# Kernel optimization log

Hardware: AMD Instinct MI355X
Metric: run time of the kernel (lower is better)

Reference implementation:

```python
import jax, jax.numpy as jnp
import numpy as np

N_NODES = 10000
N_EDGES = 160000
D = 256
L = 2
EPS = 1e-5


def setup_inputs() -> dict:
    key = jax.random.key(0)
    ks = jax.random.split(key, 12)
    s = 0.05  # weight init scale to keep activations tame
    return {
        "node_h": jax.random.normal(ks[0], (N_NODES, D), jnp.float32),
        "edge_h": jax.random.normal(ks[1], (N_EDGES, D), jnp.float32),
        "src": jax.random.randint(ks[2], (N_EDGES,), 0, N_NODES, jnp.int32),
        "dst": jax.random.randint(ks[3], (N_EDGES,), 0, N_NODES, jnp.int32),
        "Kw": jax.random.normal(ks[4], (L, 2 * D, D), jnp.float32) * s,
        "Kb": jnp.zeros((L, D), jnp.float32),
        "Vw": jax.random.normal(ks[5], (L, 2 * D, D), jnp.float32) * s,
        "Vb": jnp.zeros((L, D), jnp.float32),
        "Qw": jax.random.normal(ks[6], (L, D, D), jnp.float32) * s,
        "Qb": jnp.zeros((L, D), jnp.float32),
        "Ww": jax.random.normal(ks[7], (L, 2 * D, D), jnp.float32) * s,
        "Wb": jnp.zeros((L, D), jnp.float32),
        "Ew": jax.random.normal(ks[8], (L, 3 * D, D), jnp.float32) * s,
        "Eb": jnp.zeros((L, D), jnp.float32),
        "ln_g": jnp.ones((D,), jnp.float32),
        "ln_b": jnp.zeros((D,), jnp.float32),
    }


def _layernorm(x, g, b):
    mu = jnp.mean(x, axis=-1, keepdims=True)
    var = jnp.mean(jnp.square(x - mu), axis=-1, keepdims=True)
    return (x - mu) * jax.lax.rsqrt(var + EPS) * g + b


def _hypergraph_layer(h_n, h_e, src, dst, Kw, Kb, Vw, Vb, Qw, Qb, Ww, Wb, Ew, Eb):
    n = h_n.shape[0]
    src_h = h_n[src]                                   # [E, D] gather
    msg = jnp.concatenate([src_h * h_e, src_h], axis=1)  # [E, 2D]
    Q = h_n @ Qw + Qb                                  # [N, D]
    K = msg @ Kw + Kb                                  # [E, D]
    V = msg @ Vw + Vb                                  # [E, D]
    alpha = Q[dst] * K                                 # v_mul_e -> [E, D]
    # edge_softmax: per-destination-node, per-feature softmax over edges
    m = jax.ops.segment_max(alpha, dst, num_segments=n)
    e = jnp.exp(alpha - m[dst])
    z = jax.ops.segment_sum(e, dst, num_segments=n)
    a = e / z[dst]
    agg = jax.ops.segment_sum(a * V, dst, num_segments=n)  # sum aggregation [N, D]
    h_n_new = jnp.concatenate([agg, h_n], axis=1) @ Ww + Wb
    h_e_new = jnp.concatenate([h_n_new[src], h_n_new[dst], h_e], axis=1) @ Ew + Eb
    return h_n_new, h_e_new


def reference(node_h, edge_h, src, dst, Kw, Kb, Vw, Vb, Qw, Qb, Ww, Wb, Ew, Eb, ln_g, ln_b):
    h_n, h_e = node_h, edge_h
    for l in range(L):  # small fixed layer count
        h_n, h_e = _hypergraph_layer(h_n, h_e, src, dst,
                                     Kw[l], Kb[l], Vw[l], Vb[l], Qw[l], Qb[l],
                                     Ww[l], Wb[l], Ew[l], Eb[l])
        # relu -> layernorm; dropout is identity in eval mode
        h_n = _layernorm(jax.nn.relu(h_n), ln_g, ln_b)
        h_e = _layernorm(jax.nn.relu(h_e), ln_g, ln_b)
    return h_n, h_e
```

## Files before the change

### kernel.cpp

```cpp
#include <hip/hip_runtime.h>

#define NN 10000
#define NE 160000
#define DD 256
#define LEPS 1e-5f

typedef __attribute__((ext_vector_type(8))) short short8v;
typedef __attribute__((ext_vector_type(4))) float floatx4;
typedef unsigned short US;

static __device__ __forceinline__ US f2bf(float f){
  unsigned u = __builtin_bit_cast(unsigned, f);
  u += 0x7FFFu + ((u >> 16) & 1u);
  return (US)(u >> 16);
}
static __device__ __forceinline__ float bf2f(US s){
  unsigned u = ((unsigned)s) << 16;
  return __builtin_bit_cast(float, u);
}
template<typename T>
static __device__ __forceinline__ void ld8(const T* p, float* o){
  if constexpr (sizeof(T) == 2) {
    union { US h[8]; uint4 q; } u;
    u.q = *(const uint4*)p;
#pragma unroll
    for (int j = 0; j < 8; ++j) o[j] = bf2f(u.h[j]);
  } else {
    float4 a = *(const float4*)p; float4 b = *(const float4*)(p + 4);
    o[0]=a.x; o[1]=a.y; o[2]=a.z; o[3]=a.w; o[4]=b.x; o[5]=b.y; o[6]=b.z; o[7]=b.w;
  }
}
template<typename OT>
static __device__ __forceinline__ void st1(OT* p, float v){
  if constexpr (sizeof(OT) == 2) *p = (OT)f2bf(v); else *p = (OT)v;
}
static __device__ __forceinline__ uint4 pack8(const float* a){
  union { US h[8]; uint4 q; } pk;
#pragma unroll
  for (int j = 0; j < 8; ++j) pk.h[j] = f2bf(a[j]);
  return pk.q;
}

#define AOFF_Q  0
#define AOFF_K1 (32*2048)
#define AOFF_K2 (64*2048)
#define AOFF_V1 (96*2048)
#define AOFF_V2 (128*2048)
#define AOFF_W  (160*2048)
#define AOFF_E1 (224*2048)
#define AOFF_E2 (256*2048)
#define AOFF_E3 (288*2048)
__global__ void pack_all_k(const float* __restrict__ Qw, const float* __restrict__ Kw,
                           const float* __restrict__ Vw, const float* __restrict__ Ww,
                           const float* __restrict__ Ew, US* __restrict__ arena){
  int i = blockIdx.x * 256 + threadIdx.x;
  int g = i >> 8, n = i & 255;
  const float* src; int row0;
  if      (g <  32){ src = Qw; row0 = g*8; }
  else if (g <  64){ src = Kw; row0 = (g-32)*8; }
  else if (g <  96){ src = Kw; row0 = 256 + (g-64)*8; }
  else if (g < 128){ src = Vw; row0 = (g-96)*8; }
  else if (g < 160){ src = Vw; row0 = 256 + (g-128)*8; }
  else if (g < 224){ src = Ww; row0 = (g-160)*8; }
  else if (g < 256){ src = Ew; row0 = (g-224)*8; }
  else if (g < 288){ src = Ew; row0 = 256 + (g-256)*8; }
  else             { src = Ew; row0 = 512 + (g-288)*8; }
  union { US h[8]; uint4 q; } pk;
#pragma unroll
  for (int j = 0; j < 8; ++j) pk.h[j] = f2bf(src[(size_t)(row0 + j)*DD + n]);
  *(uint4*)(arena + (size_t)g*2048 + n*8) = pk.q;
}

template<typename AT, typename OT>
__global__ __launch_bounds__(256, 2)
void gemm_nmulti_k(const AT* __restrict__ p0,
                   const US* bp0, const float* b0, OT* o0,
                   const US* bp1, const float* b1, OT* o1,
                   const US* bp2, const float* b2, OT* o2, int M)
{
  const US* Bp  = (blockIdx.y == 0) ? bp0 : (blockIdx.y == 1 ? bp1 : bp2);
  const float* bias = (blockIdx.y == 0) ? b0 : (blockIdx.y == 1 ? b1 : b2);
  OT* out = (blockIdx.y == 0) ? o0 : (blockIdx.y == 1 ? o1 : o2);
  __shared__ __align__(16) US Alds[64][40];
  __shared__ __align__(16) US Blds[8192];
  const int tid  = threadIdx.x;
  const int lane = tid & 63;
  const int wav  = tid >> 6;
  const int bm   = blockIdx.x * 64;

  floatx4 acc[4][4];
#pragma unroll
  for (int i = 0; i < 4; ++i)
#pragma unroll
    for (int j = 0; j < 4; ++j) acc[i][j] = (floatx4){0.f,0.f,0.f,0.f};

  const int ar = tid >> 2;
  const int ak = (tid & 3) << 3;
  int grow = bm + ar; if (grow > M - 1) grow = M - 1;
  const AT* rA = p0 + (size_t)grow * DD;
  const int rq = lane >> 4;
  const int cl = lane & 15;

  uint4 arow[8];
#pragma unroll
  for (int t = 0; t < 8; ++t) {
    float av[8]; ld8(rA + t*32 + ak, av);
    arow[t] = pack8(av);
  }

  for (int t = 0; t < 8; ++t) {
    *(uint4*)&Alds[ar][ak] = arow[t];
    const uint4* bsrc = (const uint4*)(Bp + (size_t)(t*4) * 2048);
    uint4* bdst = (uint4*)Blds;
#pragma unroll
    for (int u = 0; u < 4; ++u) bdst[tid + u*256] = bsrc[tid + u*256];
    __syncthreads();

    short8v af[4], bfr[4];
#pragma unroll
    for (int i = 0; i < 4; ++i) af[i] = *(const short8v*)&Alds[i*16 + cl][rq*8];
#pragma unroll
    for (int j = 0; j < 4; ++j) bfr[j] = *(const short8v*)&Blds[(size_t)(rq*256 + wav*64 + j*16 + cl) * 8];
#pragma unroll
    for (int i = 0; i < 4; ++i)
#pragma unroll
      for (int j = 0; j < 4; ++j)
        acc[i][j] = __builtin_amdgcn_mfma_f32_16x16x32_bf16(af[i], bfr[j], acc[i][j], 0, 0, 0);
    __syncthreads();
  }

#pragma unroll
  for (int i = 0; i < 4; ++i)
#pragma unroll
    for (int r = 0; r < 4; ++r) {
      int gm = bm + i*16 + rq*4 + r;
      if (gm < M) {
#pragma unroll
        for (int j = 0; j < 4; ++j) {
          int n = wav*64 + j*16 + cl;
          float b = bias ? bias[n] : 0.f;
          st1(out + (size_t)gm*DD + n, acc[i][j][r] + b);
        }
      }
    }
}

template<typename AT, typename OT>
__global__ __launch_bounds__(256, 2)
void gemm_w_k(const float* __restrict__ p0, const AT* __restrict__ p1,
              const US* __restrict__ Bp, const float* __restrict__ bias,
              const float* __restrict__ lg, const float* __restrict__ lb,
              float* __restrict__ Craw, OT* __restrict__ Cln, int M)
{
  __shared__ __align__(16) US Alds[64][40];
  __shared__ __align__(16) US Blds[8192];
  __shared__ float S1[4][64], S2[4][64];
  const int tid  = threadIdx.x;
  const int lane = tid & 63;
  const int wav  = tid >> 6;
  const int bm   = blockIdx.x * 64;

  floatx4 acc[4][4];
#pragma unroll
  for (int i = 0; i < 4; ++i)
#pragma unroll
    for (int j = 0; j < 4; ++j) acc[i][j] = (floatx4){0.f,0.f,0.f,0.f};

  const int ar = tid >> 2;
  const int ak = (tid & 3) << 3;
  int grow = bm + ar; if (grow > M - 1) grow = M - 1;
  const float* rA = p0 + (size_t)grow * DD;
  const AT*    rB = p1 + (size_t)grow * DD;
  const int rq = lane >> 4;
  const int cl = lane & 15;

  uint4 arow[16];
#pragma unroll
  for (int t = 0; t < 16; ++t) {
    const int kk = t*32 + ak;
    float av[8];
    if (kk < DD) ld8(rA + kk, av); else ld8(rB + kk - DD, av);
    arow[t] = pack8(av);
  }

  for (int t = 0; t < 16; ++t) {
    *(uint4*)&Alds[ar][ak] = arow[t];
    const uint4* bsrc = (const uint4*)(Bp + (size_t)(t*4) * 2048);
    uint4* bdst = (uint4*)Blds;
#pragma unroll
    for (int u = 0; u < 4; ++u) bdst[tid + u*256] = bsrc[tid + u*256];
    __syncthreads();

    short8v af[4], bfr[4];
#pragma unroll
    for (int i = 0; i < 4; ++i) af[i] = *(const short8v*)&Alds[i*16 + cl][rq*8];
#pragma unroll
    for (int j = 0; j < 4; ++j) bfr[j] = *(const short8v*)&Blds[(size_t)(rq*256 + wav*64 + j*16 + cl) * 8];
#pragma unroll
    for (int i = 0; i < 4; ++i)
#pragma unroll
      for (int j = 0; j < 4; ++j)
        acc[i][j] = __builtin_amdgcn_mfma_f32_16x16x32_bf16(af[i], bfr[j], acc[i][j], 0, 0, 0);
    __syncthreads();
  }

#pragma unroll
  for (int i = 0; i < 4; ++i)
#pragma unroll
    for (int j = 0; j < 4; ++j) {
      int n = wav*64 + j*16 + cl;
      float bs = bias[n];
#pragma unroll
      for (int r = 0; r < 4; ++r) {
        int gm = bm + i*16 + rq*4 + r;
        float val = acc[i][j][r] + bs;
        if (gm < M) Craw[(size_t)gm*DD + n] = val;
        acc[i][j][r] = fmaxf(val, 0.f);
      }
    }
#pragma unroll
  for (int i = 0; i < 4; ++i)
#pragma unroll
    for (int r = 0; r < 4; ++r) {
      float s1 = 0.f, s2 = 0.f;
#pragma unroll
      for (int j = 0; j < 4; ++j){ float v = acc[i][j][r]; s1 += v; s2 += v*v; }
#pragma unroll
      for (int o = 1; o < 16; o <<= 1){ s1 += __shfl_xor(s1, o, 64); s2 += __shfl_xor(s2, o, 64); }
      if (cl == 0){ S1[wav][i*16 + rq*4 + r] = s1; S2[wav][i*16 + rq*4 + r] = s2; }
    }
  __syncthreads();
#pragma unroll
  for (int i = 0; i < 4; ++i)
#pragma unroll
    for (int r = 0; r < 4; ++r) {
      int rr = i*16 + rq*4 + r;
      float t1 = S1[0][rr] + S1[1][rr] + S1[2][rr] + S1[3][rr];
      float t2 = S2[0][rr] + S2[1][rr] + S2[2][rr] + S2[3][rr];
      float mu = t1 * (1.f/256.f);
      float var = t2 * (1.f/256.f) - mu*mu;
      float rs = rsqrtf(fmaxf(var, 0.f) + LEPS);
      int gm = bm + i*16 + rq*4 + r;
      if (gm < M) {
#pragma unroll
        for (int j = 0; j < 4; ++j) {
          int n = wav*64 + j*16 + cl;
          st1(Cln + (size_t)gm*DD + n, (acc[i][j][r] - mu) * rs * lg[n] + lb[n]);
        }
      }
    }
}

template<typename AT>
__global__ __launch_bounds__(256, 2)
void gemm_kve_k(const AT* __restrict__ p0, const AT* __restrict__ p1,
                const int* __restrict__ srcI,
                const US* __restrict__ BpK, const US* __restrict__ BpV,
                const US* __restrict__ KN, const US* __restrict__ VN,
                const int* __restrict__ eperm,
                US* __restrict__ Km, US* __restrict__ Vm, int M)
{
  __shared__ __align__(16) US Alds[64][40];
  __shared__ __align__(16) US BldsK[8192];
  __shared__ __align__(16) US BldsV[8192];
  const int tid  = threadIdx.x;
  const int lane = tid & 63;
  const int wav  = tid >> 6;
  const int bm   = blockIdx.x * 64;

  floatx4 accK[4][4], accV[4][4];
#pragma unroll
  for (int i = 0; i < 4; ++i)
#pragma unroll
    for (int j = 0; j < 4; ++j){ accK[i][j] = (floatx4){0.f,0.f,0.f,0.f}; accV[i][j] = (floatx4){0.f,0.f,0.f,0.f}; }

  const int ar = tid >> 2;
  const int ak = (tid & 3) << 3;
  int grow = bm + ar; if (grow > M - 1) grow = M - 1;
  int s = srcI[grow];
  const AT* rA = p0 + (size_t)s * DD;
  const AT* rB = p1 + (size_t)grow * DD;
  const int rq = lane >> 4;
  const int cl = lane & 15;

  uint4 msg[8];
#pragma unroll
  for (int t = 0; t < 8; ++t) {
    const int kk = t*32 + ak;
    float av[8], bv[8];
    ld8(rA + kk, av); ld8(rB + kk, bv);
    float mv[8];
#pragma unroll
    for (int j = 0; j < 8; ++j) mv[j] = av[j] * bv[j];
    msg[t] = pack8(mv);
  }

  for (int t = 0; t < 8; ++t) {
    *(uint4*)&Alds[ar][ak] = msg[t];
    const uint4* bsK = (const uint4*)(BpK + (size_t)(t*4) * 2048);
    const uint4* bsV = (const uint4*)(BpV + (size_t)(t*4) * 2048);
    uint4* bdK = (uint4*)BldsK; uint4* bdV = (uint4*)BldsV;
#pragma unroll
    for (int u = 0; u < 4; ++u){ bdK[tid + u*256] = bsK[tid + u*256]; bdV[tid + u*256] = bsV[tid + u*256]; }
    __syncthreads();

    short8v af[4], bK4[4], bV4[4];
#pragma unroll
    for (int i = 0; i < 4; ++i) af[i] = *(const short8v*)&Alds[i*16 + cl][rq*8];
#pragma unroll
    for (int j = 0; j < 4; ++j){
      size_t bi = (size_t)(rq*256 + wav*64 + j*16 + cl) * 8;
      bK4[j] = *(const short8v*)&BldsK[bi];
      bV4[j] = *(const short8v*)&BldsV[bi];
    }
#pragma unroll
    for (int i = 0; i < 4; ++i)
#pragma unroll
      for (int j = 0; j < 4; ++j){
        accK[i][j] = __builtin_amdgcn_mfma_f32_16x16x32_bf16(af[i], bK4[j], accK[i][j], 0, 0, 0);
        accV[i][j] = __builtin_amdgcn_mfma_f32_16x16x32_bf16(af[i], bV4[j], accV[i][j], 0, 0, 0);
      }
    __syncthreads();
  }

#pragma unroll
  for (int i = 0; i < 4; ++i)
#pragma unroll
    for (int r = 0; r < 4; ++r) {
      int gm = bm + i*16 + rq*4 + r;
      if (gm < M) {
        int pg = eperm[gm];
        int sg = srcI[gm];
        const US* kn = KN + (size_t)sg * DD;
        const US* vn = VN + (size_t)sg * DD;
#pragma unroll
        for (int j = 0; j < 4; ++j) {
          int n = wav*64 + j*16 + cl;
          Km[(size_t)pg*DD + n] = f2bf(accK[i][j][r] + bf2f(kn[n]));
          Vm[(size_t)pg*DD + n] = f2bf(accV[i][j][r] + bf2f(vn[n]));
        }
      }
    }
}

template<typename AT, typename OT>
__global__ __launch_bounds__(256, 2)
void gemm_e_k(const AT* __restrict__ he, const int* __restrict__ srcI,
              const int* __restrict__ dstI, const US* __restrict__ Bp,
              const US* __restrict__ EN1, const US* __restrict__ EN2,
              const float* __restrict__ lg, const float* __restrict__ lb,
              OT* __restrict__ Cln, int M)
{
  __shared__ __align__(16) US Alds[64][40];
  __shared__ __align__(16) US Blds[8192];
  __shared__ float S1[4][64], S2[4][64];
  const int tid  = threadIdx.x;
  const int lane = tid & 63;
  const int wav  = tid >> 6;
  const int bm   = blockIdx.x * 64;

  floatx4 acc[4][4];
#pragma unroll
  for (int i = 0; i < 4; ++i)
#pragma unroll
    for (int j = 0; j < 4; ++j) acc[i][j] = (floatx4){0.f,0.f,0.f,0.f};

  const int ar = tid >> 2;
  const int ak = (tid & 3) << 3;
  int grow = bm + ar; if (grow > M - 1) grow = M - 1;
  const AT* rA = he + (size_t)grow * DD;
  const int rq = lane >> 4;
  const int cl = lane & 15;

  uint4 arow[8];
#pragma unroll
  for (int t = 0; t < 8; ++t) {
    float av[8]; ld8(rA + t*32 + ak, av);
    arow[t] = pack8(av);
  }

  for (int t = 0; t < 8; ++t) {
    *(uint4*)&Alds[ar][ak] = arow[t];
    const uint4* bsrc = (const uint4*)(Bp + (size_t)(t*4) * 2048);
    uint4* bdst = (uint4*)Blds;
#pragma unroll
    for (int u = 0; u < 4; ++u) bdst[tid + u*256] = bsrc[tid + u*256];
    __syncthreads();

    short8v af[4], bfr[4];
#pragma unroll
    for (int i = 0; i < 4; ++i) af[i] = *(const short8v*)&Alds[i*16 + cl][rq*8];
#pragma unroll
    for (int j = 0; j < 4; ++j) bfr[j] = *(const short8v*)&Blds[(size_t)(rq*256 + wav*64 + j*16 + cl) * 8];
#pragma unroll
    for (int i = 0; i < 4; ++i)
#pragma unroll
      for (int j = 0; j < 4; ++j)
        acc[i][j] = __builtin_amdgcn_mfma_f32_16x16x32_bf16(af[i], bfr[j], acc[i][j], 0, 0, 0);
    __syncthreads();
  }

#pragma unroll
  for (int i = 0; i < 4; ++i)
#pragma unroll
    for (int r = 0; r < 4; ++r) {
      int gm = bm + i*16 + rq*4 + r;
      int gmc = (gm < M) ? gm : (M - 1);
      const US* e1 = EN1 + (size_t)srcI[gmc] * DD;
      const US* e2 = EN2 + (size_t)dstI[gmc] * DD;
#pragma unroll
      for (int j = 0; j < 4; ++j) {
        int n = wav*64 + j*16 + cl;
        float val = acc[i][j][r] + bf2f(e1[n]) + bf2f(e2[n]);
        acc[i][j][r] = fmaxf(val, 0.f);
      }
    }
#pragma unroll
  for (int i = 0; i < 4; ++i)
#pragma unroll
    for (int r = 0; r < 4; ++r) {
      float s1 = 0.f, s2 = 0.f;
#pragma unroll
      for (int j = 0; j < 4; ++j){ float v = acc[i][j][r]; s1 += v; s2 += v*v; }
#pragma unroll
      for (int o = 1; o < 16; o <<= 1){ s1 += __shfl_xor(s1, o, 64); s2 += __shfl_xor(s2, o, 64); }
      if (cl == 0){ S1[wav][i*16 + rq*4 + r] = s1; S2[wav][i*16 + rq*4 + r] = s2; }
    }
  __syncthreads();
#pragma unroll
  for (int i = 0; i < 4; ++i)
#pragma unroll
    for (int r = 0; r < 4; ++r) {
      int rr = i*16 + rq*4 + r;
      float t1 = S1[0][rr] + S1[1][rr] + S1[2][rr] + S1[3][rr];
      float t2 = S2[0][rr] + S2[1][rr] + S2[2][rr] + S2[3][rr];
      float mu = t1 * (1.f/256.f);
      float var = t2 * (1.f/256.f) - mu*mu;
      float rs = rsqrtf(fmaxf(var, 0.f) + LEPS);
      int gm = bm + i*16 + rq*4 + r;
      if (gm < M) {
#pragma unroll
        for (int j = 0; j < 4; ++j) {
          int n = wav*64 + j*16 + cl;
          st1(Cln + (size_t)gm*DD + n, (acc[i][j][r] - mu) * rs * lg[n] + lb[n]);
        }
      }
    }
}

__global__ void count_k(const int* __restrict__ dst, int* __restrict__ cnt, int e){
  int i = blockIdx.x * blockDim.x + threadIdx.x;
  if (i < e) atomicAdd(&cnt[dst[i]], 1);
}
__global__ void scan_k(const int* __restrict__ cnt, int* __restrict__ rp, int n){
  __shared__ int part[256];
  const int t = threadIdx.x;
  const int chunk = (n + 255) / 256;
  int lo = t * chunk, hi = lo + chunk; if (hi > n) hi = n; if (lo > n) lo = n;
  int s = 0;
  for (int i = lo; i < hi; ++i) s += cnt[i];
  part[t] = s; __syncthreads();
  if (t == 0){ int run = 0; for (int i = 0; i < 256; ++i){ int tmp = part[i]; part[i] = run; run += tmp; } rp[n] = run; }
  __syncthreads();
  int run = part[t];
  for (int i = lo; i < hi; ++i){ rp[i] = run; run += cnt[i]; }
}
__global__ void scatter_k(const int* __restrict__ dst, const int* __restrict__ rp,
                          int* __restrict__ pos, int* __restrict__ eperm, int e){
  int i = blockIdx.x * blockDim.x + threadIdx.x;
  if (i >= e) return;
  int d = dst[i];
  int p = atomicAdd(&pos[d], 1);
  eperm[i] = rp[d] + p;
}

__global__ __launch_bounds__(256)
void node_agg_k(const int* __restrict__ rp,
                const US* __restrict__ Q, const US* __restrict__ Km,
                const US* __restrict__ Vm, float* __restrict__ agg)
{
  int d = blockIdx.x, f = threadIdx.x;
  int beg = rp[d], end = rp[d + 1];
  float q = bf2f(Q[(size_t)d * DD + f]);
  float m = -3.0e38f, z = 0.f, s = 0.f;
  for (int i = beg; i < end; ++i){
    float a  = q * bf2f(Km[(size_t)i * DD + f]);
    float vv = bf2f(Vm[(size_t)i * DD + f]);
    float mn = fmaxf(m, a);
    float sc = __expf(m - mn);
    float w  = __expf(a - mn);
    z = z * sc + w;
    s = s * sc + w * vv;
    m = mn;
  }
  agg[(size_t)d * DD + f] = (z > 0.f) ? (s / z) : 0.f;
}

__global__ void sentinel_k(int hostbits, float* out){
  int code = 0;
  if (hostbits & 1) code = 1;
  else if (hostbits & 2) code = 2;
  else if (hostbits & 4) code = 3;
  else if (hostbits & 8) code = 4;
  if (code) out[0] = (float)code * 1.0e6f;
}

struct Bufs {
  float *agg, *hn_new;
  US *QN, *KN, *VN, *EN1, *EN2, *Kmat, *Vmat, *arena;
  int *rp, *eperm;
  const int *src, *dst;
  const float *lg, *lb;
};
template<typename AT, typename OT>
static void layer_run(const Bufs& B, const AT* hn_in, const AT* he_in,
                      OT* hn_out, OT* he_out,
                      const float* Kb, const float* Vb, const float* Qb,
                      const float* Wb, const float* Eb, hipStream_t stream)
{
  const int gN = (NN + 63) / 64, gE = (NE + 63) / 64;
  gemm_nmulti_k<AT, US><<<dim3(gN, 3), 256, 0, stream>>>(hn_in,
      B.arena + AOFF_Q, Qb, B.QN,
      B.arena + AOFF_K2, Kb, B.KN,
      B.arena + AOFF_V2, Vb, B.VN, NN);
  gemm_kve_k<AT><<<gE, 256, 0, stream>>>(hn_in, he_in, B.src,
      B.arena + AOFF_K1, B.arena + AOFF_V1, B.KN, B.VN, B.eperm, B.Kmat, B.Vmat, NE);
  node_agg_k<<<NN, 256, 0, stream>>>(B.rp, B.QN, B.Kmat, B.Vmat, B.agg);
  gemm_w_k<AT, OT><<<gN, 256, 0, stream>>>(B.agg, hn_in, B.arena + AOFF_W, Wb,
      B.lg, B.lb, B.hn_new, hn_out, NN);
  gemm_nmulti_k<float, US><<<dim3(gN, 2), 256, 0, stream>>>(B.hn_new,
      B.arena + AOFF_E1, Eb, B.EN1,  B.arena + AOFF_E2, nullptr, B.EN2,
      B.arena + AOFF_E2, nullptr, B.EN2, NN);
  gemm_e_k<AT, OT><<<gE, 256, 0, stream>>>(he_in, B.src, B.dst, B.arena + AOFF_E3,
      B.EN1, B.EN2, B.lg, B.lb, he_out, NE);
}

extern "C" void kernel_launch(void* const* d_in, const int* in_sizes, int n_in,
                              void* d_out, int out_size, void* d_ws, size_t ws_size,
                              hipStream_t stream) {
  const float* node_h = (const float*)d_in[0];
  const float* edge_h = (const float*)d_in[1];
  const int*   src    = (const int*)d_in[2];
  const int*   dst    = (const int*)d_in[3];
  const float* Kw = (const float*)d_in[4];  const float* Kb = (const float*)d_in[5];
  const float* Vw = (const float*)d_in[6];  const float* Vb = (const float*)d_in[7];
  const float* Qw = (const float*)d_in[8];  const float* Qb = (const float*)d_in[9];
  const float* Ww = (const float*)d_in[10]; const float* Wb = (const float*)d_in[11];
  const float* Ew = (const float*)d_in[12]; const float* Eb = (const float*)d_in[13];
  const float* ln_g = (const float*)d_in[14];
  const float* ln_b = (const float*)d_in[15];

  char* w = (char*)d_ws; size_t off = 0;
  auto alloc = [&](size_t bytes)->char* {
    char* p = w + off; off += (bytes + 255) & ~(size_t)255; return p;
  };
  float* agg    = (float*)alloc((size_t)NN * DD * 4);
  float* hn_new = (float*)alloc((size_t)NN * DD * 4);
  US* QN     = (US*)alloc((size_t)NN * DD * 2);
  US* hn_cur = (US*)alloc((size_t)NN * DD * 2);
  US* KN     = (US*)alloc((size_t)NN * DD * 2);
  US* VN     = (US*)alloc((size_t)NN * DD * 2);
  US* EN1    = (US*)alloc((size_t)NN * DD * 2);
  US* EN2    = (US*)alloc((size_t)NN * DD * 2);
  US* Kmat   = (US*)alloc((size_t)NE * DD * 2);
  US* Vmat   = (US*)alloc((size_t)NE * DD * 2);
  US* he_cur = (US*)alloc((size_t)NE * DD * 2);
  US* arena  = (US*)alloc((size_t)320 * 2048 * 2);
  int* cnt   = (int*)alloc((size_t)NN * 4);
  int* rp    = (int*)alloc((size_t)(NN + 1) * 4);
  int* pos   = (int*)alloc((size_t)NN * 4);
  int* eperm = (int*)alloc((size_t)NE * 4);

  float* out_hn = (float*)d_out;
  float* out_he = out_hn + (size_t)NN * DD;

  int hostbits = 0;
  {
    static const int exp_sizes[16] = {NN*DD, NE*DD, NE, NE, 2*512*DD, 2*DD, 2*512*DD, 2*DD,
                                      2*DD*DD, 2*DD, 2*512*DD, 2*DD, 2*768*DD, 2*DD, DD, DD};
    if (n_in != 16) hostbits |= 2;
    else { for (int i = 0; i < 16; ++i) if (in_sizes[i] != exp_sizes[i]) hostbits |= 2; }
    if (out_size != NN*DD + NE*DD) hostbits |= 4;
    if (off > ws_size) hostbits |= 1;
  }
  if (hostbits) {
    sentinel_k<<<1, 1, 0, stream>>>(hostbits, out_hn);
    return;
  }

  hipMemsetAsync(cnt, 0, (size_t)NN * 4, stream);
  hipMemsetAsync(pos, 0, (size_t)NN * 4, stream);
  count_k<<<(NE + 255)/256, 256, 0, stream>>>(dst, cnt, NE);
  scan_k<<<1, 256, 0, stream>>>(cnt, rp, NN);
  scatter_k<<<(NE + 255)/256, 256, 0, stream>>>(dst, rp, pos, eperm, NE);

  Bufs B{agg, hn_new, QN, KN, VN, EN1, EN2, Kmat, Vmat, arena, rp, eperm, src, dst, ln_g, ln_b};

  pack_all_k<<<320, 256, 0, stream>>>(Qw, Kw, Vw, Ww, Ew, arena);
  layer_run<float, US>(B, node_h, edge_h, hn_cur, he_cur,
                       Kb, Vb, Qb, Wb, Eb, stream);
  pack_all_k<<<320, 256, 0, stream>>>(Qw + (size_t)256*DD, Kw + (size_t)512*DD,
                                      Vw + (size_t)512*DD, Ww + (size_t)512*DD,
                                      Ew + (size_t)768*DD, arena);
  layer_run<US, float>(B, hn_cur, he_cur, out_hn, out_he,
                       Kb + DD, Vb + DD, Qb + DD, Wb + DD, Eb + DD, stream);

  if (hipGetLastError() != hipSuccess) {
    sentinel_k<<<1, 1, 0, stream>>>(8, out_hn);
  }
}
```

Baseline: 901.3 us.

## Process K/V edge GEMM rows in source-sorted order for gather locality

Adds a second counting sort that groups edge indices by source node (esrc), and the K/V GEMM now takes its rows in that order. Edges sharing a source node then sit in the same tile, so the gathers of node features and KN/VN rows should hit cache more often. The price is an indirect, non-coalesced read of edge_h rows, plus extra sort kernels and memsets. It also drops the register staging of all eight message chunks and computes each chunk inside the k-loop, which lowers register pressure but exposes the global load latency.

```diff
diff --git a/kernel.cpp b/kernel.cpp
--- a/kernel.cpp
+++ b/kernel.cpp
@@ -254,7 +254,7 @@
 template<typename AT>
 __global__ __launch_bounds__(256, 2)
 void gemm_kve_k(const AT* __restrict__ p0, const AT* __restrict__ p1,
-                const int* __restrict__ srcI,
+                const int* __restrict__ srcI, const int* __restrict__ esrc,
                 const US* __restrict__ BpK, const US* __restrict__ BpV,
                 const US* __restrict__ KN, const US* __restrict__ VN,
                 const int* __restrict__ eperm,
@@ -277,14 +277,13 @@
   const int ar = tid >> 2;
   const int ak = (tid & 3) << 3;
   int grow = bm + ar; if (grow > M - 1) grow = M - 1;
-  int s = srcI[grow];
+  int e = esrc[grow];
+  int s = srcI[e];
   const AT* rA = p0 + (size_t)s * DD;
-  const AT* rB = p1 + (size_t)grow * DD;
+  const AT* rB = p1 + (size_t)e * DD;
   const int rq = lane >> 4;
   const int cl = lane & 15;
 
-  uint4 msg[8];
-#pragma unroll
   for (int t = 0; t < 8; ++t) {
     const int kk = t*32 + ak;
     float av[8], bv[8];
@@ -292,11 +291,8 @@
     float mv[8];
 #pragma unroll
     for (int j = 0; j < 8; ++j) mv[j] = av[j] * bv[j];
-    msg[t] = pack8(mv);
-  }
-
-  for (int t = 0; t < 8; ++t) {
-    *(uint4*)&Alds[ar][ak] = msg[t];
+    *(uint4*)&Alds[ar][ak] = pack8(mv);
+
     const uint4* bsK = (const uint4*)(BpK + (size_t)(t*4) * 2048);
     const uint4* bsV = (const uint4*)(BpV + (size_t)(t*4) * 2048);
     uint4* bdK = (uint4*)BldsK; uint4* bdV = (uint4*)BldsV;
@@ -329,8 +325,9 @@
     for (int r = 0; r < 4; ++r) {
       int gm = bm + i*16 + rq*4 + r;
       if (gm < M) {
-        int pg = eperm[gm];
-        int sg = srcI[gm];
+        int eg = esrc[gm];
+        int pg = eperm[eg];
+        int sg = srcI[eg];
         const US* kn = KN + (size_t)sg * DD;
         const US* vn = VN + (size_t)sg * DD;
 #pragma unroll
@@ -448,9 +445,9 @@
     }
 }
 
-__global__ void count_k(const int* __restrict__ dst, int* __restrict__ cnt, int e){
+__global__ void count_k(const int* __restrict__ key, int* __restrict__ cnt, int e){
   int i = blockIdx.x * blockDim.x + threadIdx.x;
-  if (i < e) atomicAdd(&cnt[dst[i]], 1);
+  if (i < e) atomicAdd(&cnt[key[i]], 1);
 }
 __global__ void scan_k(const int* __restrict__ cnt, int* __restrict__ rp, int n){
   __shared__ int part[256];
@@ -465,13 +462,21 @@
   int run = part[t];
   for (int i = lo; i < hi; ++i){ rp[i] = run; run += cnt[i]; }
 }
-__global__ void scatter_k(const int* __restrict__ dst, const int* __restrict__ rp,
+__global__ void scatter_k(const int* __restrict__ key, const int* __restrict__ rp,
                           int* __restrict__ pos, int* __restrict__ eperm, int e){
   int i = blockIdx.x * blockDim.x + threadIdx.x;
   if (i >= e) return;
-  int d = dst[i];
+  int d = key[i];
   int p = atomicAdd(&pos[d], 1);
   eperm[i] = rp[d] + p;
+}
+__global__ void scatter_col_k(const int* __restrict__ key, const int* __restrict__ rp,
+                              int* __restrict__ pos, int* __restrict__ col, int e){
+  int i = blockIdx.x * blockDim.x + threadIdx.x;
+  if (i >= e) return;
+  int d = key[i];
+  int p = atomicAdd(&pos[d], 1);
+  col[rp[d] + p] = i;
 }
 
 __global__ __launch_bounds__(256)
@@ -508,7 +513,7 @@
 struct Bufs {
   float *agg, *hn_new;
   US *QN, *KN, *VN, *EN1, *EN2, *Kmat, *Vmat, *arena;
-  int *rp, *eperm;
+  int *rp, *eperm, *esrc;
   const int *src, *dst;
   const float *lg, *lb;
 };
@@ -523,7 +528,7 @@
       B.arena + AOFF_Q, Qb, B.QN,
       B.arena + AOFF_K2, Kb, B.KN,
       B.arena + AOFF_V2, Vb, B.VN, NN);
-  gemm_kve_k<AT><<<gE, 256, 0, stream>>>(hn_in, he_in, B.src,
+  gemm_kve_k<AT><<<gE, 256, 0, stream>>>(hn_in, he_in, B.src, B.esrc,
       B.arena + AOFF_K1, B.arena + AOFF_V1, B.KN, B.VN, B.eperm, B.Kmat, B.Vmat, NE);
   node_agg_k<<<NN, 256, 0, stream>>>(B.rp, B.QN, B.Kmat, B.Vmat, B.agg);
   gemm_w_k<AT, OT><<<gN, 256, 0, stream>>>(B.agg, hn_in, B.arena + AOFF_W, Wb,
@@ -568,8 +573,10 @@
   US* arena  = (US*)alloc((size_t)320 * 2048 * 2);
   int* cnt   = (int*)alloc((size_t)NN * 4);
   int* rp    = (int*)alloc((size_t)(NN + 1) * 4);
+  int* rpS   = (int*)alloc((size_t)(NN + 1) * 4);
   int* pos   = (int*)alloc((size_t)NN * 4);
   int* eperm = (int*)alloc((size_t)NE * 4);
+  int* esrc  = (int*)alloc((size_t)NE * 4);
 
   float* out_hn = (float*)d_out;
   float* out_he = out_hn + (size_t)NN * DD;
@@ -593,8 +600,14 @@
   count_k<<<(NE + 255)/256, 256, 0, stream>>>(dst, cnt, NE);
   scan_k<<<1, 256, 0, stream>>>(cnt, rp, NN);
   scatter_k<<<(NE + 255)/256, 256, 0, stream>>>(dst, rp, pos, eperm, NE);
-
-  Bufs B{agg, hn_new, QN, KN, VN, EN1, EN2, Kmat, Vmat, arena, rp, eperm, src, dst, ln_g, ln_b};
+  hipMemsetAsync(cnt, 0, (size_t)NN * 4, stream);
+  hipMemsetAsync(pos, 0, (size_t)NN * 4, stream);
+  count_k<<<(NE + 255)/256, 256, 0, stream>>>(src, cnt, NE);
+  scan_k<<<1, 256, 0, stream>>>(cnt, rpS, NN);
+  scatter_col_k<<<(NE + 255)/256, 256, 0, stream>>>(src, rpS, pos, esrc, NE);
+
+  Bufs B{agg, hn_new, QN, KN, VN, EN1, EN2, Kmat, Vmat, arena, rp, eperm, esrc,
+         src, dst, ln_g, ln_b};
 
   pack_all_k<<<320, 256, 0, stream>>>(Qw, Kw, Vw, Ww, Ew, arena);
   layer_run<float, US>(B, node_h, edge_h, hn_cur, he_cur,
```

After: 930.5 us. 1.03x slower.
